# Kernel tuning notes

Measured on AMD Instinct MI355X. Metric: run time of the kernel, lower is better.

## Reference

```python
import jax, jax.numpy as jnp
import numpy as np

B, N, M, D, F, H = 8, 512, 512, 512, 512, 8
D_H, F_H = D // H, F // H


def setup_inputs() -> dict:
    key = jax.random.key(0)
    ks = jax.random.split(key, 7)
    X = jax.random.normal(ks[0], (B, N, D), dtype=jnp.float32)
    V = jax.random.normal(ks[1], (B, M, F), dtype=jnp.float32)
    # learned parameters, init normal(0, 0.02) as in the torch module
    W_Q_1 = 0.02 * jax.random.normal(ks[2], (H, N, D_H, D_H), dtype=jnp.float32)
    W_Q_2 = 0.02 * jax.random.normal(ks[3], (H, N, M, D_H), dtype=jnp.float32)
    W_V = 0.02 * jax.random.normal(ks[4], (H, F_H, F_H), dtype=jnp.float32)
    O_w = 0.02 * jax.random.normal(ks[5], (F, F), dtype=jnp.float32)
    O_b = jnp.zeros((F,), dtype=jnp.float32)
    return {"X": X, "V": V, "W_Q_1": W_Q_1, "W_Q_2": W_Q_2,
            "W_V": W_V, "O_w": O_w, "O_b": O_b}


def reference(X, V, W_Q_1, W_Q_2, W_V, O_w, O_b):
    b, n, d = X.shape
    _, m, f = V.shape
    Xh = X.reshape(b, n, H, d // H)      # [B,N,H,D_H]
    Vh = V.reshape(b, m, H, f // H)      # [B,M,H,F_H]
    # 'hndd' repeats d within one operand -> diagonal of W_Q_1's last two dims
    # (faithful to torch.einsum semantics): per-position per-channel scale.
    Q_1 = jnp.einsum('bnhd,hndd->bhnd', Xh, W_Q_1)
    Q_1 = jax.nn.gelu(Q_1, approximate=False)  # torch nn.GELU default = exact erf
    Q_2 = jnp.einsum('bhnd,hnmd->bhnm', Q_1, W_Q_2)  # synthesized attention logits
    A = jax.nn.softmax(Q_2, axis=3)                  # softmax over M
    # 'hff' likewise takes the diagonal of W_V -> per-head channel scale fused
    # with the attention-weighted value aggregation.
    Y = jnp.einsum('bhnm,bmhf,hff->bnhf', A, Vh, W_V)
    Y = Y.reshape(b, n, f)
    return Y @ O_w.T + O_b
```

## Files before the change

kernel.cpp:

```cpp
#include <hip/hip_runtime.h>
#include <cstdint>

#define B_ 8
#define N_ 512
#define M_ 512
#define D_ 512
#define F_ 512
#define H_ 8
#define DH_ 64
#define FH_ 64

typedef __attribute__((ext_vector_type(8))) short bf16x8;
typedef __attribute__((ext_vector_type(4))) float f32x4;
typedef __attribute__((ext_vector_type(8))) unsigned short u16x8;

__device__ __forceinline__ unsigned short f2bf(float x) {
    unsigned u = __float_as_uint(x);
    return (unsigned short)((u + 0x7fffu + ((u >> 16) & 1u)) >> 16);
}
__device__ __forceinline__ float bf2f(unsigned short b) {
    return __uint_as_float(((unsigned)b) << 16);
}

__device__ __forceinline__ f32x4 ntload4(const float* p) {
    return __builtin_nontemporal_load((const f32x4*)p);
}
__device__ __forceinline__ float ntload1(const float* p) {
    return __builtin_nontemporal_load(p);
}

template <int CTRL>
__device__ __forceinline__ float dpp_add(float x) {
    int y = __builtin_amdgcn_update_dpp(0, __float_as_int(x), CTRL, 0xf, 0xf, true);
    return x + __int_as_float(y);
}

__global__ __launch_bounds__(256, 4) void syn_k_attn(const float* __restrict__ X,
                                                     const float* __restrict__ W1,
                                                     const float* __restrict__ W2,
                                                     unsigned short* __restrict__ Ahi) {
    int hn = blockIdx.x;
    int h = hn >> 9, n = hn & 511;
    int t = threadIdx.x;
    int wave = t >> 6, lane = t & 63;
    __shared__ float q1s[8 * 68];
    __shared__ float logits[8 * 520];

    {
        int d = t & 63;
        int b0 = t >> 6;
        float w = ntload1(W1 + (size_t)hn * (DH_ * DH_) + d * (DH_ + 1));
        #pragma unroll
        for (int i = 0; i < 2; ++i) {
            int bi = b0 + i * 4;
            float x = X[((size_t)(bi * N_ + n)) * D_ + h * DH_ + d];
            float v = x * w;
            q1s[bi * 68 + d] = 0.5f * v * (1.0f + erff(v * 0.70710678118654752440f));
        }
    }
    __syncthreads();

    int mr = lane >> 3, c = lane & 7;
    float4 qa[8], qb[8];
    #pragma unroll
    for (int b = 0; b < 8; ++b) {
        qa[b] = *(const float4*)&q1s[b * 68 + c * 8];
        qb[b] = *(const float4*)&q1s[b * 68 + c * 8 + 4];
    }

    const float* w2 = W2 + (size_t)hn * ((size_t)M_ * DH_);
    #pragma unroll 4
    for (int g = 0; g < 16; ++g) {
        int m = (wave + g * 4) * 8 + mr;
        const float* wr = w2 + (size_t)m * DH_ + c * 8;
        f32x4 wa = ntload4(wr);
        f32x4 wb = ntload4(wr + 4);
        float acc[8];
        #pragma unroll
        for (int b = 0; b < 8; ++b) {
            float a0 = wa.x * qa[b].x + wa.y * qa[b].y + wa.z * qa[b].z + wa.w * qa[b].w
                     + wb.x * qb[b].x + wb.y * qb[b].y + wb.z * qb[b].z + wb.w * qb[b].w;
            a0 = dpp_add<0xB1>(a0);
            a0 = dpp_add<0x4E>(a0);
            a0 = dpp_add<0x124>(a0);
            acc[b] = a0;
        }
        float lo = c == 0 ? acc[0] : c == 1 ? acc[1] : c == 2 ? acc[2] : acc[3];
        float hi = c == 0 ? acc[4] : c == 1 ? acc[5] : c == 2 ? acc[6] : acc[7];
        if (c < 4) {
            logits[c * 520 + m] = lo;
            logits[(c + 4) * 520 + m] = hi;
        }
    }
    __syncthreads();

    for (int bb = wave; bb < 8; bb += 4) {
        const float* lrow = &logits[bb * 520 + lane * 8];
        float4 va = *(const float4*)lrow;
        float4 vb = *(const float4*)(lrow + 4);
        float v[8] = {va.x, va.y, va.z, va.w, vb.x, vb.y, vb.z, vb.w};
        float mx = v[0];
        #pragma unroll
        for (int i = 1; i < 8; ++i) mx = fmaxf(mx, v[i]);
        #pragma unroll
        for (int s = 1; s < 64; s <<= 1) mx = fmaxf(mx, __shfl_xor(mx, s));
        float e[8]; float sum = 0.f;
        #pragma unroll
        for (int i = 0; i < 8; ++i) { e[i] = expf(v[i] - mx); sum += e[i]; }
        #pragma unroll
        for (int s = 1; s < 64; s <<= 1) sum += __shfl_xor(sum, s);
        float inv = 1.0f / sum;
        unsigned short hb[8];
        #pragma unroll
        for (int i = 0; i < 8; ++i) hb[i] = f2bf(e[i] * inv);
        size_t base = ((size_t)(bb * H_ + h) * N_ + n) * M_ + lane * 8;
        *(u16x8*)(Ahi + base) = *(u16x8*)hb;
    }
}

__global__ __launch_bounds__(256) void syn_k_splitw(const float* __restrict__ Ow,
                                                    unsigned short* __restrict__ Whi,
                                                    unsigned short* __restrict__ Wlo) {
    int i = (blockIdx.x * 256 + threadIdx.x) * 4;
    float4 v = *(const float4*)(Ow + i);
    float vv[4] = {v.x, v.y, v.z, v.w};
    unsigned short hb[4], lb[4];
    #pragma unroll
    for (int j = 0; j < 4; ++j) {
        hb[j] = f2bf(vv[j]);
        lb[j] = f2bf(vv[j] - bf2f(hb[j]));
    }
    uint2 hv, lv;
    hv.x = (unsigned)hb[0] | ((unsigned)hb[1] << 16);
    hv.y = (unsigned)hb[2] | ((unsigned)hb[3] << 16);
    lv.x = (unsigned)lb[0] | ((unsigned)lb[1] << 16);
    lv.y = (unsigned)lb[2] | ((unsigned)lb[3] << 16);
    *(uint2*)(Whi + i) = hv;
    *(uint2*)(Wlo + i) = lv;
}

__global__ __launch_bounds__(256) void syn_k_splitv(const float* __restrict__ V,
                                                    unsigned short* __restrict__ Vthi) {
    int bh = blockIdx.x;
    int b = bh >> 3, h = bh & 7;
    int t = threadIdx.x;
    __shared__ float lds[64 * 68];
    for (int m0 = 0; m0 < M_; m0 += 64) {
        int m = t >> 2, fo = (t & 3) * 16;
        const float* src = V + ((size_t)(b * M_ + m0 + m)) * F_ + h * FH_ + fo;
        #pragma unroll
        for (int i = 0; i < 4; ++i)
            *(float4*)&lds[m * 68 + fo + i * 4] = *(const float4*)(src + i * 4);
        __syncthreads();
        int f = t >> 2, mo = (t & 3) * 16;
        unsigned short hb[16];
        #pragma unroll
        for (int i = 0; i < 16; ++i)
            hb[i] = f2bf(lds[(mo + i) * 68 + f]);
        size_t base = ((size_t)(bh * 64 + f)) * 512 + m0 + mo;
        *(u16x8*)(Vthi + base) = *(u16x8*)hb;
        *(u16x8*)(Vthi + base + 8) = *(u16x8*)&hb[8];
        __syncthreads();
    }
}

__global__ __launch_bounds__(256) void syn_k_pv_mfma(const unsigned short* __restrict__ Ahi,
                                                     const unsigned short* __restrict__ Vthi,
                                                     const float* __restrict__ WV,
                                                     unsigned short* __restrict__ Yhi,
                                                     unsigned short* __restrict__ Ylo) {
    int bh = blockIdx.y;
    int b = bh >> 3, h = bh & 7;
    int n0 = blockIdx.x * 32;
    int t = threadIdx.x;
    int lane = t & 63, wave = t >> 6;
    int wr = wave >> 1, wc = wave & 1;
    __shared__ __align__(16) unsigned short Alh[32 * 64];
    __shared__ __align__(16) unsigned short Blh[64 * 64];
    f32x4 acc[2];
    acc[0] = (f32x4){0.f, 0.f, 0.f, 0.f};
    acc[1] = (f32x4){0.f, 0.f, 0.f, 0.f};

    int srow = t >> 3, skg = t & 7;
    int sslot = skg ^ (srow & 7);
    const unsigned short* Ahb = Ahi + ((size_t)bh * N_ + n0) * M_;
    const unsigned short* Vhb = Vthi + ((size_t)bh * 64) * 512;

    u16x8 rAh, rBh0, rBh1;
    {
        rAh  = *(const u16x8*)(Ahb + (size_t)srow * M_ + skg * 8);
        rBh0 = *(const u16x8*)(Vhb + (size_t)srow * 512 + skg * 8);
        rBh1 = *(const u16x8*)(Vhb + (size_t)(srow + 32) * 512 + skg * 8);
    }

    #pragma unroll 1
    for (int mb = 0; mb < 8; ++mb) {
        *(u16x8*)&Alh[srow * 64 + sslot * 8] = rAh;
        *(u16x8*)&Blh[srow * 64 + sslot * 8] = rBh0;
        *(u16x8*)&Blh[(srow + 32) * 64 + sslot * 8] = rBh1;
        __syncthreads();
        if (mb < 7) {
            int m0 = (mb + 1) * 64;
            rAh  = *(const u16x8*)(Ahb + (size_t)srow * M_ + m0 + skg * 8);
            rBh0 = *(const u16x8*)(Vhb + (size_t)srow * 512 + m0 + skg * 8);
            rBh1 = *(const u16x8*)(Vhb + (size_t)(srow + 32) * 512 + m0 + skg * 8);
        }
        #pragma unroll
        for (int mg = 0; mg < 2; ++mg) {
            int kslot = (mg * 4 + (lane >> 4)) ^ (lane & 7);
            int arow = wr * 16 + (lane & 15);
            bf16x8 afh = *(const bf16x8*)&Alh[arow * 64 + kslot * 8];
            #pragma unroll
            for (int j = 0; j < 2; ++j) {
                int brow = wc * 32 + j * 16 + (lane & 15);
                bf16x8 bfh = *(const bf16x8*)&Blh[brow * 64 + kslot * 8];
                acc[j] = __builtin_amdgcn_mfma_f32_16x16x32_bf16(afh, bfh, acc[j], 0, 0, 0);
            }
        }
        __syncthreads();
    }

    int crow = n0 + wr * 16 + (lane >> 4) * 4;
    int ccol = wc * 32 + (lane & 15);
    #pragma unroll
    for (int j = 0; j < 2; ++j) {
        int f = ccol + j * 16;
        float s = WV[(size_t)h * (FH_ * FH_) + f * (FH_ + 1)];
        #pragma unroll
        for (int r = 0; r < 4; ++r) {
            int row = crow + r;
            float y = acc[j][r] * s;
            unsigned short hb = f2bf(y);
            unsigned short lb = f2bf(y - bf2f(hb));
            size_t base = ((size_t)(b * N_ + row)) * F_ + h * FH_ + f;
            Yhi[base] = hb;
            Ylo[base] = lb;
        }
    }
}

__global__ __launch_bounds__(256) void syn_k_out_mfma(const unsigned short* __restrict__ Yhi,
                                                      const unsigned short* __restrict__ Ylo,
                                                      const unsigned short* __restrict__ Whi,
                                                      const unsigned short* __restrict__ Wlo,
                                                      const float* __restrict__ Ob,
                                                      float* __restrict__ out) {
    int r0 = blockIdx.x * 64;
    int f0 = blockIdx.y * 64;
    int t = threadIdx.x;
    int lane = t & 63, wave = t >> 6;
    int wr = wave >> 1, wc = wave & 1;
    __shared__ __align__(16) unsigned short Alh[64 * 64], All[64 * 64];
    __shared__ __align__(16) unsigned short Blh[64 * 64], Bll[64 * 64];
    f32x4 acc[2][2];
    #pragma unroll
    for (int i = 0; i < 2; ++i)
        #pragma unroll
        for (int j = 0; j < 2; ++j) acc[i][j] = (f32x4){0.f, 0.f, 0.f, 0.f};

    int srow = t >> 3, skg = t & 7;
    int sslot = skg ^ (srow & 7);

    #pragma unroll 1
    for (int kb = 0; kb < 512; kb += 64) {
        #pragma unroll
        for (int rr = 0; rr < 2; ++rr) {
            int row = srow + rr * 32;
            size_t ya = (size_t)(r0 + row) * 512 + kb + skg * 8;
            size_t wa = (size_t)(f0 + row) * 512 + kb + skg * 8;
            *(u16x8*)&Alh[row * 64 + sslot * 8] = *(const u16x8*)(Yhi + ya);
            *(u16x8*)&All[row * 64 + sslot * 8] = *(const u16x8*)(Ylo + ya);
            *(u16x8*)&Blh[row * 64 + sslot * 8] = *(const u16x8*)(Whi + wa);
            *(u16x8*)&Bll[row * 64 + sslot * 8] = *(const u16x8*)(Wlo + wa);
        }
        __syncthreads();
        #pragma unroll
        for (int mg = 0; mg < 2; ++mg) {
            int kslot = (mg * 4 + (lane >> 4)) ^ (lane & 7);
            bf16x8 afh[2], afl[2], bfh[2], bfl[2];
            #pragma unroll
            for (int q = 0; q < 2; ++q) {
                int arow = wr * 32 + q * 16 + (lane & 15);
                afh[q] = *(const bf16x8*)&Alh[arow * 64 + kslot * 8];
                afl[q] = *(const bf16x8*)&All[arow * 64 + kslot * 8];
                int brow = wc * 32 + q * 16 + (lane & 15);
                bfh[q] = *(const bf16x8*)&Blh[brow * 64 + kslot * 8];
                bfl[q] = *(const bf16x8*)&Bll[brow * 64 + kslot * 8];
            }
            #pragma unroll
            for (int i = 0; i < 2; ++i)
                #pragma unroll
                for (int j = 0; j < 2; ++j) {
                    acc[i][j] = __builtin_amdgcn_mfma_f32_16x16x32_bf16(afh[i], bfh[j], acc[i][j], 0, 0, 0);
                    acc[i][j] = __builtin_amdgcn_mfma_f32_16x16x32_bf16(afh[i], bfl[j], acc[i][j], 0, 0, 0);
                    acc[i][j] = __builtin_amdgcn_mfma_f32_16x16x32_bf16(afl[i], bfh[j], acc[i][j], 0, 0, 0);
                }
        }
        __syncthreads();
    }

    int crow = r0 + wr * 32 + (lane >> 4) * 4;
    int ccol = f0 + wc * 32 + (lane & 15);
    float ob0 = Ob[ccol], ob1 = Ob[ccol + 16];
    #pragma unroll
    for (int i = 0; i < 2; ++i)
        #pragma unroll
        for (int j = 0; j < 2; ++j) {
            float obv = (j == 0) ? ob0 : ob1;
            #pragma unroll
            for (int r = 0; r < 4; ++r) {
                int row = crow + i * 16 + r;
                out[(size_t)row * F_ + ccol + j * 16] = acc[i][j][r] + obv;
            }
        }
}

extern "C" void kernel_launch(void* const* d_in, const int* in_sizes, int n_in,
                              void* d_out, int out_size, void* d_ws, size_t ws_size,
                              hipStream_t stream) {
    const float* X  = (const float*)d_in[0];
    const float* V  = (const float*)d_in[1];
    const float* W1 = (const float*)d_in[2];
    const float* W2 = (const float*)d_in[3];
    const float* WV = (const float*)d_in[4];
    const float* Ow = (const float*)d_in[5];
    const float* Ob = (const float*)d_in[6];
    float* out = (float*)d_out;

    unsigned short* Ahi = (unsigned short*)d_ws;
    unsigned short* Yhi = Ahi + (size_t)B_ * H_ * N_ * M_;
    unsigned short* Ylo = Yhi + (size_t)B_ * N_ * F_;
    unsigned short* Whi = Ylo + (size_t)B_ * N_ * F_;
    unsigned short* Wlo = Whi + (size_t)F_ * F_;
    unsigned short* Vthi = Wlo + (size_t)F_ * F_;

    syn_k_splitw<<<(F_ * F_) / (256 * 4), 256, 0, stream>>>(Ow, Whi, Wlo);
    syn_k_splitv<<<B_ * H_, 256, 0, stream>>>(V, Vthi);
    syn_k_attn<<<H_ * N_, 256, 0, stream>>>(X, W1, W2, Ahi);
    syn_k_pv_mfma<<<dim3(N_ / 32, B_ * H_), 256, 0, stream>>>(Ahi, Vthi, WV, Yhi, Ylo);
    syn_k_out_mfma<<<dim3((B_ * N_) / 64, F_ / 64), 256, 0, stream>>>(Yhi, Ylo, Whi, Wlo, Ob, out);
}
```

Baseline: 169.5 us.

## Fuse softmax attention with PV MFMA to drop the materialized attention matrix

Merges the attention-logit/softmax kernel with the PV matmul kernel. Each block now handles two query positions for one head across all batches: it keeps the bf16 softmax probabilities in LDS and runs MFMA directly against transposed V read from global memory. This removes the 32 MB bf16 attention buffer write and read, plus one kernel launch. In exchange, every block re-reads the head's full transposed V slice from cache, and most MFMA output columns are redundant because only one row group is stored. LDS use per block also grows.

```diff
diff --git a/kernel.cpp b/kernel.cpp
--- a/kernel.cpp
+++ b/kernel.cpp
@@ -35,86 +35,149 @@
     return x + __int_as_float(y);
 }
 
-__global__ __launch_bounds__(256, 4) void syn_k_attn(const float* __restrict__ X,
-                                                     const float* __restrict__ W1,
-                                                     const float* __restrict__ W2,
-                                                     unsigned short* __restrict__ Ahi) {
-    int hn = blockIdx.x;
-    int h = hn >> 9, n = hn & 511;
+__global__ __launch_bounds__(256, 4) void syn_k_attn_pv(const float* __restrict__ X,
+                                                        const float* __restrict__ W1,
+                                                        const float* __restrict__ W2,
+                                                        const unsigned short* __restrict__ Vthi,
+                                                        const float* __restrict__ WV,
+                                                        unsigned short* __restrict__ Yhi,
+                                                        unsigned short* __restrict__ Ylo) {
+    int bid = blockIdx.x;
+    int h = bid & 7;
+    int n0 = (bid >> 3) * 2;
     int t = threadIdx.x;
     int wave = t >> 6, lane = t & 63;
-    __shared__ float q1s[8 * 68];
+    __shared__ float q1s[2][8 * 68];
     __shared__ float logits[8 * 520];
+    __shared__ __align__(16) unsigned short pbf[2][8 * 512];
 
     {
-        int d = t & 63;
-        int b0 = t >> 6;
-        float w = ntload1(W1 + (size_t)hn * (DH_ * DH_) + d * (DH_ + 1));
-        #pragma unroll
-        for (int i = 0; i < 2; ++i) {
-            int bi = b0 + i * 4;
-            float x = X[((size_t)(bi * N_ + n)) * D_ + h * DH_ + d];
-            float v = x * w;
-            q1s[bi * 68 + d] = 0.5f * v * (1.0f + erff(v * 0.70710678118654752440f));
+        int d = t & 63, b0 = t >> 6;
+        #pragma unroll
+        for (int nq = 0; nq < 2; ++nq) {
+            int n = n0 + nq;
+            int hn = h * 512 + n;
+            float w = ntload1(W1 + (size_t)hn * (DH_ * DH_) + d * (DH_ + 1));
+            #pragma unroll
+            for (int i = 0; i < 2; ++i) {
+                int bi = b0 + i * 4;
+                float x = X[((size_t)(bi * N_ + n)) * D_ + h * DH_ + d];
+                float v = x * w;
+                q1s[nq][bi * 68 + d] = 0.5f * v * (1.0f + erff(v * 0.70710678118654752440f));
+            }
         }
     }
     __syncthreads();
 
     int mr = lane >> 3, c = lane & 7;
-    float4 qa[8], qb[8];
-    #pragma unroll
-    for (int b = 0; b < 8; ++b) {
-        qa[b] = *(const float4*)&q1s[b * 68 + c * 8];
-        qb[b] = *(const float4*)&q1s[b * 68 + c * 8 + 4];
-    }
-
-    const float* w2 = W2 + (size_t)hn * ((size_t)M_ * DH_);
-    #pragma unroll 4
-    for (int g = 0; g < 16; ++g) {
-        int m = (wave + g * 4) * 8 + mr;
-        const float* wr = w2 + (size_t)m * DH_ + c * 8;
-        f32x4 wa = ntload4(wr);
-        f32x4 wb = ntload4(wr + 4);
-        float acc[8];
+    #pragma unroll 1
+    for (int nq = 0; nq < 2; ++nq) {
+        int hn = h * 512 + n0 + nq;
+        float4 qa[8], qb[8];
         #pragma unroll
         for (int b = 0; b < 8; ++b) {
-            float a0 = wa.x * qa[b].x + wa.y * qa[b].y + wa.z * qa[b].z + wa.w * qa[b].w
-                     + wb.x * qb[b].x + wb.y * qb[b].y + wb.z * qb[b].z + wb.w * qb[b].w;
-            a0 = dpp_add<0xB1>(a0);
-            a0 = dpp_add<0x4E>(a0);
-            a0 = dpp_add<0x124>(a0);
-            acc[b] = a0;
-        }
-        float lo = c == 0 ? acc[0] : c == 1 ? acc[1] : c == 2 ? acc[2] : acc[3];
-        float hi = c == 0 ? acc[4] : c == 1 ? acc[5] : c == 2 ? acc[6] : acc[7];
-        if (c < 4) {
-            logits[c * 520 + m] = lo;
-            logits[(c + 4) * 520 + m] = hi;
-        }
-    }
-    __syncthreads();
-
-    for (int bb = wave; bb < 8; bb += 4) {
-        const float* lrow = &logits[bb * 520 + lane * 8];
-        float4 va = *(const float4*)lrow;
-        float4 vb = *(const float4*)(lrow + 4);
-        float v[8] = {va.x, va.y, va.z, va.w, vb.x, vb.y, vb.z, vb.w};
-        float mx = v[0];
-        #pragma unroll
-        for (int i = 1; i < 8; ++i) mx = fmaxf(mx, v[i]);
-        #pragma unroll
-        for (int s = 1; s < 64; s <<= 1) mx = fmaxf(mx, __shfl_xor(mx, s));
-        float e[8]; float sum = 0.f;
-        #pragma unroll
-        for (int i = 0; i < 8; ++i) { e[i] = expf(v[i] - mx); sum += e[i]; }
-        #pragma unroll
-        for (int s = 1; s < 64; s <<= 1) sum += __shfl_xor(sum, s);
-        float inv = 1.0f / sum;
-        unsigned short hb[8];
-        #pragma unroll
-        for (int i = 0; i < 8; ++i) hb[i] = f2bf(e[i] * inv);
-        size_t base = ((size_t)(bb * H_ + h) * N_ + n) * M_ + lane * 8;
-        *(u16x8*)(Ahi + base) = *(u16x8*)hb;
+            qa[b] = *(const float4*)&q1s[nq][b * 68 + c * 8];
+            qb[b] = *(const float4*)&q1s[nq][b * 68 + c * 8 + 4];
+        }
+        const float* w2 = W2 + (size_t)hn * ((size_t)M_ * DH_);
+        #pragma unroll 4
+        for (int g = 0; g < 16; ++g) {
+            int m = (wave + g * 4) * 8 + mr;
+            const float* wr = w2 + (size_t)m * DH_ + c * 8;
+            f32x4 wa = ntload4(wr);
+            f32x4 wb = ntload4(wr + 4);
+            float acc[8];
+            #pragma unroll
+            for (int b = 0; b < 8; ++b) {
+                float a0 = wa.x * qa[b].x + wa.y * qa[b].y + wa.z * qa[b].z + wa.w * qa[b].w
+                         + wb.x * qb[b].x + wb.y * qb[b].y + wb.z * qb[b].z + wb.w * qb[b].w;
+                a0 = dpp_add<0xB1>(a0);
+                a0 = dpp_add<0x4E>(a0);
+                a0 = dpp_add<0x124>(a0);
+                acc[b] = a0;
+            }
+            float lo = c == 0 ? acc[0] : c == 1 ? acc[1] : c == 2 ? acc[2] : acc[3];
+            float hi = c == 0 ? acc[4] : c == 1 ? acc[5] : c == 2 ? acc[6] : acc[7];
+            if (c < 4) {
+                logits[c * 520 + m] = lo;
+                logits[(c + 4) * 520 + m] = hi;
+            }
+        }
+        __syncthreads();
+
+        for (int bb = wave; bb < 8; bb += 4) {
+            const float* lrow = &logits[bb * 520 + lane * 8];
+            float4 va = *(const float4*)lrow;
+            float4 vb = *(const float4*)(lrow + 4);
+            float v[8] = {va.x, va.y, va.z, va.w, vb.x, vb.y, vb.z, vb.w};
+            float mx = v[0];
+            #pragma unroll
+            for (int i = 1; i < 8; ++i) mx = fmaxf(mx, v[i]);
+            #pragma unroll
+            for (int s = 1; s < 64; s <<= 1) mx = fmaxf(mx, __shfl_xor(mx, s));
+            float e[8]; float sum = 0.f;
+            #pragma unroll
+            for (int i = 0; i < 8; ++i) { e[i] = expf(v[i] - mx); sum += e[i]; }
+            #pragma unroll
+            for (int s = 1; s < 64; s <<= 1) sum += __shfl_xor(sum, s);
+            float inv = 1.0f / sum;
+            unsigned short hb[8];
+            #pragma unroll
+            for (int i = 0; i < 8; ++i) hb[i] = f2bf(e[i] * inv);
+            *(u16x8*)&pbf[nq][bb * 512 + lane * 8] = *(u16x8*)hb;
+        }
+        __syncthreads();
+    }
+
+    int ft = wave;
+    int frow = lane & 15, kg = lane >> 4;
+    float sv[4];
+    #pragma unroll
+    for (int r = 0; r < 4; ++r)
+        sv[r] = WV[(size_t)h * (FH_ * FH_) + (ft * 16 + kg * 4 + r) * (FH_ + 1)];
+
+    #pragma unroll
+    for (int b2 = 0; b2 < 2; ++b2) {
+        f32x4 acc[4][2];
+        #pragma unroll
+        for (int b4 = 0; b4 < 4; ++b4)
+            #pragma unroll
+            for (int q = 0; q < 2; ++q)
+                acc[b4][q] = (f32x4){0.f, 0.f, 0.f, 0.f};
+
+        #pragma unroll
+        for (int b4 = 0; b4 < 4; ++b4) {
+            int b = b2 * 4 + b4;
+            const unsigned short* vt = Vthi
+                + ((size_t)((b * 8 + h) * 64 + ft * 16 + frow)) * 512 + kg * 8;
+            const unsigned short* p0 = &pbf[0][b * 512 + kg * 8];
+            const unsigned short* p1 = &pbf[1][b * 512 + kg * 8];
+            #pragma unroll 4
+            for (int ks = 0; ks < 16; ++ks) {
+                bf16x8 av  = *(const bf16x8*)(vt + ks * 32);
+                bf16x8 pb0 = *(const bf16x8*)(p0 + ks * 32);
+                bf16x8 pb1 = *(const bf16x8*)(p1 + ks * 32);
+                acc[b4][0] = __builtin_amdgcn_mfma_f32_16x16x32_bf16(av, pb0, acc[b4][0], 0, 0, 0);
+                acc[b4][1] = __builtin_amdgcn_mfma_f32_16x16x32_bf16(av, pb1, acc[b4][1], 0, 0, 0);
+            }
+        }
+        if (frow == 0) {
+            #pragma unroll
+            for (int b4 = 0; b4 < 4; ++b4)
+                #pragma unroll
+                for (int nq = 0; nq < 2; ++nq)
+                    #pragma unroll
+                    for (int r = 0; r < 4; ++r) {
+                        int f = ft * 16 + kg * 4 + r;
+                        float y = acc[b4][nq][r] * sv[r];
+                        unsigned short hbb = f2bf(y);
+                        unsigned short lbb = f2bf(y - bf2f(hbb));
+                        int b = b2 * 4 + b4;
+                        size_t base = ((size_t)(b * N_ + n0 + nq)) * F_ + h * FH_ + f;
+                        Yhi[base] = hbb;
+                        Ylo[base] = lbb;
+                    }
+        }
     }
 }
 
@@ -161,81 +224,6 @@
         *(u16x8*)(Vthi + base) = *(u16x8*)hb;
         *(u16x8*)(Vthi + base + 8) = *(u16x8*)&hb[8];
         __syncthreads();
-    }
-}
-
-__global__ __launch_bounds__(256) void syn_k_pv_mfma(const unsigned short* __restrict__ Ahi,
-                                                     const unsigned short* __restrict__ Vthi,
-                                                     const float* __restrict__ WV,
-                                                     unsigned short* __restrict__ Yhi,
-                                                     unsigned short* __restrict__ Ylo) {
-    int bh = blockIdx.y;
-    int b = bh >> 3, h = bh & 7;
-    int n0 = blockIdx.x * 32;
-    int t = threadIdx.x;
-    int lane = t & 63, wave = t >> 6;
-    int wr = wave >> 1, wc = wave & 1;
-    __shared__ __align__(16) unsigned short Alh[32 * 64];
-    __shared__ __align__(16) unsigned short Blh[64 * 64];
-    f32x4 acc[2];
-    acc[0] = (f32x4){0.f, 0.f, 0.f, 0.f};
-    acc[1] = (f32x4){0.f, 0.f, 0.f, 0.f};
-
-    int srow = t >> 3, skg = t & 7;
-    int sslot = skg ^ (srow & 7);
-    const unsigned short* Ahb = Ahi + ((size_t)bh * N_ + n0) * M_;
-    const unsigned short* Vhb = Vthi + ((size_t)bh * 64) * 512;
-
-    u16x8 rAh, rBh0, rBh1;
-    {
-        rAh  = *(const u16x8*)(Ahb + (size_t)srow * M_ + skg * 8);
-        rBh0 = *(const u16x8*)(Vhb + (size_t)srow * 512 + skg * 8);
-        rBh1 = *(const u16x8*)(Vhb + (size_t)(srow + 32) * 512 + skg * 8);
-    }
-
-    #pragma unroll 1
-    for (int mb = 0; mb < 8; ++mb) {
-        *(u16x8*)&Alh[srow * 64 + sslot * 8] = rAh;
-        *(u16x8*)&Blh[srow * 64 + sslot * 8] = rBh0;
-        *(u16x8*)&Blh[(srow + 32) * 64 + sslot * 8] = rBh1;
-        __syncthreads();
-        if (mb < 7) {
-            int m0 = (mb + 1) * 64;
-            rAh  = *(const u16x8*)(Ahb + (size_t)srow * M_ + m0 + skg * 8);
-            rBh0 = *(const u16x8*)(Vhb + (size_t)srow * 512 + m0 + skg * 8);
-            rBh1 = *(const u16x8*)(Vhb + (size_t)(srow + 32) * 512 + m0 + skg * 8);
-        }
-        #pragma unroll
-        for (int mg = 0; mg < 2; ++mg) {
-            int kslot = (mg * 4 + (lane >> 4)) ^ (lane & 7);
-            int arow = wr * 16 + (lane & 15);
-            bf16x8 afh = *(const bf16x8*)&Alh[arow * 64 + kslot * 8];
-            #pragma unroll
-            for (int j = 0; j < 2; ++j) {
-                int brow = wc * 32 + j * 16 + (lane & 15);
-                bf16x8 bfh = *(const bf16x8*)&Blh[brow * 64 + kslot * 8];
-                acc[j] = __builtin_amdgcn_mfma_f32_16x16x32_bf16(afh, bfh, acc[j], 0, 0, 0);
-            }
-        }
-        __syncthreads();
-    }
-
-    int crow = n0 + wr * 16 + (lane >> 4) * 4;
-    int ccol = wc * 32 + (lane & 15);
-    #pragma unroll
-    for (int j = 0; j < 2; ++j) {
-        int f = ccol + j * 16;
-        float s = WV[(size_t)h * (FH_ * FH_) + f * (FH_ + 1)];
-        #pragma unroll
-        for (int r = 0; r < 4; ++r) {
-            int row = crow + r;
-            float y = acc[j][r] * s;
-            unsigned short hb = f2bf(y);
-            unsigned short lb = f2bf(y - bf2f(hb));
-            size_t base = ((size_t)(b * N_ + row)) * F_ + h * FH_ + f;
-            Yhi[base] = hb;
-            Ylo[base] = lb;
-        }
     }
 }
 
@@ -327,8 +315,7 @@
     const float* Ob = (const float*)d_in[6];
     float* out = (float*)d_out;
 
-    unsigned short* Ahi = (unsigned short*)d_ws;
-    unsigned short* Yhi = Ahi + (size_t)B_ * H_ * N_ * M_;
+    unsigned short* Yhi = (unsigned short*)d_ws;
     unsigned short* Ylo = Yhi + (size_t)B_ * N_ * F_;
     unsigned short* Whi = Ylo + (size_t)B_ * N_ * F_;
     unsigned short* Wlo = Whi + (size_t)F_ * F_;
@@ -336,7 +323,6 @@
 
     syn_k_splitw<<<(F_ * F_) / (256 * 4), 256, 0, stream>>>(Ow, Whi, Wlo);
     syn_k_splitv<<<B_ * H_, 256, 0, stream>>>(V, Vthi);
-    syn_k_attn<<<H_ * N_, 256, 0, stream>>>(X, W1, W2, Ahi);
-    syn_k_pv_mfma<<<dim3(N_ / 32, B_ * H_), 256, 0, stream>>>(Ahi, Vthi, WV, Yhi, Ylo);
+    syn_k_attn_pv<<<(H_ * N_) / 2, 256, 0, stream>>>(X, W1, W2, Vthi, WV, Yhi, Ylo);
     syn_k_out_mfma<<<dim3((B_ * N_) / 64, F_ / 64), 256, 0, stream>>>(Yhi, Ylo, Whi, Wlo, Ob, out);
 }
```

Result: slower. 250.0 us (+47.5%).
